# Kernel optimization log

Hardware: AMD Instinct MI355X
Metric: run time of the kernel (lower is better)

## Reference

```python
import jax, jax.numpy as jnp
import numpy as np

N = 8192
IN_F = 256
OUT_F = 128

def setup_inputs() -> dict:
    key = jax.random.key(0)
    k1, k2, k3, k4, k5 = jax.random.split(key, 5)
    adjacency_matrix = jax.random.uniform(k1, (N, N), dtype=jnp.float32)
    node_features = jax.random.normal(k2, (N, IN_F), dtype=jnp.float32)
    # nn.Linear(in_features, out_features): W is [out, in], b is [out]
    W = jax.random.normal(k3, (OUT_F, IN_F), dtype=jnp.float32) / np.sqrt(IN_F)
    b = jax.random.normal(k4, (OUT_F,), dtype=jnp.float32) * 0.01
    attn_weights = jax.random.normal(k5, (OUT_F, OUT_F), dtype=jnp.float32)
    return {"adjacency_matrix": adjacency_matrix, "node_features": node_features,
            "W": W, "b": b, "attn_weights": attn_weights}

def reference(adjacency_matrix, node_features, W, b, attn_weights):
    # h = Linear(node_features): [N, out]
    h = node_features @ W.T + b
    # bilinear scores: h @ (A @ h^T) -> [N, N]
    scores = jnp.einsum('nd,de,me->nm', h, attn_weights, h)
    attn = jax.nn.softmax(scores, axis=1)
    # weighted aggregation: [N, N] @ [N, out]
    h_agg = attn @ h
    return h_agg
```

## Files before the change

### kernel.cpp

```cpp
#include <hip/hip_runtime.h>
#include <hip/hip_bf16.h>
#include <stdint.h>


#define NN 8192
#define INF_ 256
#define D 128
#define BQ 128
#define BK 64
#define KSPLIT 8
#define KSEG (NN / KSPLIT)
#define L2E 1.44269504088896340736f

typedef __attribute__((ext_vector_type(8))) short bf16x8;
typedef __attribute__((ext_vector_type(4))) short bf16x4;
typedef __attribute__((ext_vector_type(4))) float f32x4;
typedef __attribute__((ext_vector_type(4))) unsigned int uint4v;

__global__ __launch_bounds__(256) void prep_kernel(
    const float* __restrict__ X, const float* __restrict__ W,
    const float* __restrict__ bias, const float* __restrict__ A,
    __hip_bfloat16* __restrict__ h_hi, __hip_bfloat16* __restrict__ h_lo,
    __hip_bfloat16* __restrict__ q_hi, __hip_bfloat16* __restrict__ q_lo,
    __hip_bfloat16* __restrict__ ht)
{
    __shared__ float xs[32][INF_];
    __shared__ float hs[32][D];
    const int tid  = threadIdx.x;
    const int row0 = blockIdx.x * 32;

    {
        const f32x4* Xv = (const f32x4*)(X + (size_t)row0 * INF_);
        f32x4* xsv = (f32x4*)&xs[0][0];
        #pragma unroll
        for (int i = 0; i < 8; ++i) xsv[tid + i*256] = Xv[tid + i*256];
    }
    __syncthreads();

    const int c  = tid & 127;
    const int rh = tid >> 7;

    float acc[16];
    #pragma unroll
    for (int r = 0; r < 16; ++r) acc[r] = 0.f;
    const f32x4* Wv = (const f32x4*)(W + (size_t)c * INF_);
    for (int k4 = 0; k4 < INF_/4; ++k4) {
        f32x4 w4 = Wv[k4];
        #pragma unroll
        for (int r = 0; r < 16; ++r) {
            f32x4 x4 = ((const f32x4*)&xs[rh*16 + r][0])[k4];
            acc[r] += x4[0]*w4[0] + x4[1]*w4[1] + x4[2]*w4[2] + x4[3]*w4[3];
        }
    }
    const float bc = bias[c];
    #pragma unroll
    for (int r = 0; r < 16; ++r) {
        const int row = rh*16 + r;
        const float hv = acc[r] + bc;
        hs[row][c] = hv;
        const __hip_bfloat16 hi = __float2bfloat16(hv);
        const float lo = hv - __bfloat162float(hi);
        h_hi[(size_t)(row0+row)*D + c] = hi;
        h_lo[(size_t)(row0+row)*D + c] = __float2bfloat16(lo);
        ht  [(size_t)c*NN + row0 + row] = hi;
    }
    __syncthreads();

    float acc2[16];
    #pragma unroll
    for (int r = 0; r < 16; ++r) acc2[r] = 0.f;
    for (int d4 = 0; d4 < D/4; ++d4) {
        f32x4 hv4[16];
        #pragma unroll
        for (int r = 0; r < 16; ++r) hv4[r] = ((const f32x4*)&hs[rh*16 + r][0])[d4];
        #pragma unroll
        for (int dd = 0; dd < 4; ++dd) {
            const float a = A[(size_t)(d4*4 + dd)*D + c];
            #pragma unroll
            for (int r = 0; r < 16; ++r) acc2[r] += hv4[r][dd] * a;
        }
    }
    #pragma unroll
    for (int r = 0; r < 16; ++r) {
        const int row = rh*16 + r;
        const float tv = acc2[r];
        const __hip_bfloat16 hi = __float2bfloat16(tv);
        const float lo = tv - __bfloat162float(hi);
        q_hi[(size_t)(row0+row)*D + c] = hi;
        q_lo[(size_t)(row0+row)*D + c] = __float2bfloat16(lo);
    }
}

__global__ __launch_bounds__(256, 2) void flash_kernel(
    const __hip_bfloat16* __restrict__ q_hi, const __hip_bfloat16* __restrict__ q_lo,
    const __hip_bfloat16* __restrict__ k_hi, const __hip_bfloat16* __restrict__ k_lo,
    const __hip_bfloat16* __restrict__ ht,
    float* __restrict__ opart, float* __restrict__ mpart, float* __restrict__ lpart)
{
    __shared__ __hip_bfloat16 khi[BK][136];
    __shared__ __hip_bfloat16 klo[BK][136];
    __shared__ __hip_bfloat16 vt[D][72];

    const int tid  = threadIdx.x;
    const int wave = tid >> 6;
    const int lane = tid & 63;
    const int l16  = lane & 15;
    const int quad = lane >> 4;
    const int q0    = blockIdx.x * BQ;
    const int split = blockIdx.y;
    const int jbase = split * KSEG;

    bf16x8 bqh[2][4], bql[2][4];
    #pragma unroll
    for (int it = 0; it < 2; ++it) {
        const size_t qrow = (size_t)q0 + wave*32 + it*16 + l16;
        const __hip_bfloat16* qhp = q_hi + qrow*D;
        const __hip_bfloat16* qlp = q_lo + qrow*D;
        #pragma unroll
        for (int t = 0; t < 4; ++t) {
            bqh[it][t] = *(const bf16x8*)(qhp + t*32 + quad*8);
            bql[it][t] = *(const bf16x8*)(qlp + t*32 + quad*8);
        }
    }

    f32x4 oacc[2][8];
    #pragma unroll
    for (int it = 0; it < 2; ++it)
        #pragma unroll
        for (int i = 0; i < 8; ++i) oacc[it][i] = (f32x4){0.f, 0.f, 0.f, 0.f};
    float mi[2] = {-1e30f, -1e30f}, li[2] = {0.f, 0.f};

    for (int tile = 0; tile < KSEG/BK; ++tile) {
        const int j0 = jbase + tile * BK;
        __syncthreads();
        #pragma unroll
        for (int i = 0; i < 4; ++i) {
            const int chunk = tid + i*256;
            const int r  = chunk >> 4, c8 = chunk & 15;
            *(uint4v*)(&khi[r][c8*8]) = *(const uint4v*)(k_hi + (size_t)(j0+r)*D + c8*8);
            *(uint4v*)(&klo[r][c8*8]) = *(const uint4v*)(k_lo + (size_t)(j0+r)*D + c8*8);
            const int dd = chunk >> 3, cc = chunk & 7;
            *(uint4v*)(&vt[dd][cc*8]) = *(const uint4v*)(ht + (size_t)dd*NN + j0 + cc*8);
        }
        __syncthreads();

        f32x4 st[2][4];
        #pragma unroll
        for (int jt = 0; jt < 4; ++jt) {
            #pragma unroll
            for (int t = 0; t < 4; ++t) {
                const bf16x8 ah = *(const bf16x8*)(&khi[jt*16 + l16][t*32 + quad*8]);
                const bf16x8 al = *(const bf16x8*)(&klo[jt*16 + l16][t*32 + quad*8]);
                #pragma unroll
                for (int it = 0; it < 2; ++it) {
                    f32x4 acc = (t == 0) ? (f32x4){0.f,0.f,0.f,0.f} : st[it][jt];
                    acc = __builtin_amdgcn_mfma_f32_16x16x32_bf16(ah, bql[it][t], acc, 0, 0, 0);
                    acc = __builtin_amdgcn_mfma_f32_16x16x32_bf16(al, bqh[it][t], acc, 0, 0, 0);
                    acc = __builtin_amdgcn_mfma_f32_16x16x32_bf16(ah, bqh[it][t], acc, 0, 0, 0);
                    st[it][jt] = acc;
                }
            }
        }

        bf16x8 pb[2][2];
        #pragma unroll
        for (int it = 0; it < 2; ++it) {
            float vmax = st[it][0][0];
            #pragma unroll
            for (int jt = 0; jt < 4; ++jt)
                #pragma unroll
                for (int r = 0; r < 4; ++r) vmax = fmaxf(vmax, st[it][jt][r]);
            vmax = fmaxf(vmax, __shfl_xor(vmax, 16, 64));
            vmax = fmaxf(vmax, __shfl_xor(vmax, 32, 64));
            const float mnew  = fmaxf(mi[it], vmax);
            const float alpha = exp2f((mi[it] - mnew) * L2E);
            mi[it] = mnew;
            float sum = 0.f;
            #pragma unroll
            for (int jt = 0; jt < 4; ++jt)
                #pragma unroll
                for (int r = 0; r < 4; ++r) {
                    const float pv = exp2f((st[it][jt][r] - mnew) * L2E);
                    st[it][jt][r] = pv;
                    sum += pv;
                }
            sum += __shfl_xor(sum, 16, 64);
            sum += __shfl_xor(sum, 32, 64);
            li[it] = li[it] * alpha + sum;

            #pragma unroll
            for (int r = 0; r < 4; ++r) {
                const float ar = __shfl(alpha, quad*4 + r, 64);
                #pragma unroll
                for (int dt = 0; dt < 8; ++dt) oacc[it][dt][r] *= ar;
            }
            #pragma unroll
            for (int jp = 0; jp < 2; ++jp) {
                bf16x8 f;
                #pragma unroll
                for (int r = 0; r < 4; ++r) {
                    f[r]     = __bfloat16_as_short(__float2bfloat16(st[it][2*jp  ][r]));
                    f[r + 4] = __bfloat16_as_short(__float2bfloat16(st[it][2*jp+1][r]));
                }
                pb[it][jp] = f;
            }
        }

        #pragma unroll
        for (int dt = 0; dt < 8; ++dt) {
            const __hip_bfloat16* vrow = &vt[dt*16 + l16][0];
            #pragma unroll
            for (int jp = 0; jp < 2; ++jp) {
                const bf16x4 v0 = *(const bf16x4*)(vrow + (2*jp)*16   + quad*4);
                const bf16x4 v1 = *(const bf16x4*)(vrow + (2*jp+1)*16 + quad*4);
                bf16x8 bv;
                #pragma unroll
                for (int r = 0; r < 4; ++r) { bv[r] = v0[r]; bv[r+4] = v1[r]; }
                #pragma unroll
                for (int it = 0; it < 2; ++it)
                    oacc[it][dt] = __builtin_amdgcn_mfma_f32_16x16x32_bf16(
                        pb[it][jp], bv, oacc[it][dt], 0, 0, 0);
            }
        }
    }

    float* op = opart + ((size_t)split * NN + q0 + wave*32) * D;
    #pragma unroll
    for (int it = 0; it < 2; ++it) {
        #pragma unroll
        for (int r = 0; r < 4; ++r) {
            const int m = it*16 + quad*4 + r;
            #pragma unroll
            for (int dt = 0; dt < 8; ++dt)
                op[(size_t)m*D + dt*16 + l16] = oacc[it][dt][r];
        }
        if (quad == 0) {
            mpart[(size_t)split*NN + q0 + wave*32 + it*16 + l16] = mi[it];
            lpart[(size_t)split*NN + q0 + wave*32 + it*16 + l16] = li[it];
        }
    }
}

__global__ __launch_bounds__(256) void combine_kernel(
    const float* __restrict__ opart, const float* __restrict__ mpart,
    const float* __restrict__ lpart, float* __restrict__ out)
{
    const int idx = blockIdx.x * 256 + threadIdx.x;
    const int q = idx >> 7;
    float m = -1e30f;
    #pragma unroll
    for (int s = 0; s < KSPLIT; ++s) m = fmaxf(m, mpart[(size_t)s*NN + q]);
    float z = 0.f, o = 0.f;
    #pragma unroll
    for (int s = 0; s < KSPLIT; ++s) {
        const float w = exp2f((mpart[(size_t)s*NN + q] - m) * L2E);
        z += lpart[(size_t)s*NN + q] * w;
        o += opart[(size_t)s*NN*D + idx] * w;
    }
    out[idx] = o / z;
}

extern "C" void kernel_launch(void* const* d_in, const int* in_sizes, int n_in,
                              void* d_out, int out_size, void* d_ws, size_t ws_size,
                              hipStream_t stream)
{
    const float* X = (const float*)d_in[1];
    const float* W = (const float*)d_in[2];
    const float* b = (const float*)d_in[3];
    const float* A = (const float*)d_in[4];
    float* out = (float*)d_out;

    char* ws = (char*)d_ws;
    __hip_bfloat16* h_hi = (__hip_bfloat16*)(ws);
    __hip_bfloat16* h_lo = (__hip_bfloat16*)(ws + (size_t)(2u  << 20));
    __hip_bfloat16* q_hi = (__hip_bfloat16*)(ws + (size_t)(4u  << 20));
    __hip_bfloat16* q_lo = (__hip_bfloat16*)(ws + (size_t)(6u  << 20));
    __hip_bfloat16* ht   = (__hip_bfloat16*)(ws + (size_t)(8u  << 20));
    float* opart = (float*)(ws + (size_t)(10u << 20));
    float* mpart = (float*)(ws + (size_t)(42u << 20));
    float* lpart = (float*)(ws + (size_t)(42u << 20) + (256u << 10));

    prep_kernel<<<NN/32, 256, 0, stream>>>(X, W, b, A, h_hi, h_lo, q_hi, q_lo, ht);
    flash_kernel<<<dim3(NN/BQ, KSPLIT), 256, 0, stream>>>(
        q_hi, q_lo, h_hi, h_lo, ht, opart, mpart, lpart);
    combine_kernel<<<(NN*D)/256, 256, 0, stream>>>(opart, mpart, lpart, out);
}
```

Measured before the change: 462.0 us.

## Prefetch next K/V tile into registers, permute V layout, remap block order

The flash kernel now loads the next K/V tile from global memory into registers while the current tile is being computed, hiding global load latency behind the MFMA work. The transposed V buffer is stored in a permuted column order, so each lane's PV operand becomes one contiguous 16-byte LDS read instead of two 8-byte reads plus a shuffle. The grid is flattened with split as the fastest-varying index, so neighbouring blocks share query rows, which may improve L2 locality. The cost is extra register pressure from the prefetch buffers, which could hurt occupancy at 2 blocks per CU.

```diff
diff --git a/kernel.cpp b/kernel.cpp
--- a/kernel.cpp
+++ b/kernel.cpp
@@ -10,19 +10,24 @@
 #define BK 64
 #define KSPLIT 8
 #define KSEG (NN / KSPLIT)
+#define NTILE (KSEG / BK)
 #define L2E 1.44269504088896340736f
 
 typedef __attribute__((ext_vector_type(8))) short bf16x8;
-typedef __attribute__((ext_vector_type(4))) short bf16x4;
 typedef __attribute__((ext_vector_type(4))) float f32x4;
 typedef __attribute__((ext_vector_type(4))) unsigned int uint4v;
+
+__device__ __forceinline__ int pv_perm(int g) {
+    const int jt = (g >> 4) & 3, q = (g >> 2) & 3, r = g & 3;
+    return (g & ~63) | ((jt >> 1) * 32 + q * 8 + (jt & 1) * 4 + r);
+}
 
 __global__ __launch_bounds__(256) void prep_kernel(
     const float* __restrict__ X, const float* __restrict__ W,
     const float* __restrict__ bias, const float* __restrict__ A,
     __hip_bfloat16* __restrict__ h_hi, __hip_bfloat16* __restrict__ h_lo,
     __hip_bfloat16* __restrict__ q_hi, __hip_bfloat16* __restrict__ q_lo,
-    __hip_bfloat16* __restrict__ ht)
+    __hip_bfloat16* __restrict__ htp)
 {
     __shared__ float xs[32][INF_];
     __shared__ float hs[32][D];
@@ -62,7 +67,7 @@
         const float lo = hv - __bfloat162float(hi);
         h_hi[(size_t)(row0+row)*D + c] = hi;
         h_lo[(size_t)(row0+row)*D + c] = __float2bfloat16(lo);
-        ht  [(size_t)c*NN + row0 + row] = hi;
+        htp [(size_t)c*NN + pv_perm(row0 + row)] = hi;
     }
     __syncthreads();
 
@@ -94,7 +99,7 @@
 __global__ __launch_bounds__(256, 2) void flash_kernel(
     const __hip_bfloat16* __restrict__ q_hi, const __hip_bfloat16* __restrict__ q_lo,
     const __hip_bfloat16* __restrict__ k_hi, const __hip_bfloat16* __restrict__ k_lo,
-    const __hip_bfloat16* __restrict__ ht,
+    const __hip_bfloat16* __restrict__ htp,
     float* __restrict__ opart, float* __restrict__ mpart, float* __restrict__ lpart)
 {
     __shared__ __hip_bfloat16 khi[BK][136];
@@ -106,9 +111,23 @@
     const int lane = tid & 63;
     const int l16  = lane & 15;
     const int quad = lane >> 4;
-    const int q0    = blockIdx.x * BQ;
-    const int split = blockIdx.y;
+    const int bid   = blockIdx.x;
+    const int split = bid & 7;
+    const int q0    = (bid >> 3) * BQ;
     const int jbase = split * KSEG;
+
+    int gko[4], gvo[4], lko[4], lvo[4];
+    #pragma unroll
+    for (int i = 0; i < 4; ++i) {
+        const int chunk = tid + i*256;
+        gko[i] = (chunk >> 4) * D  + (chunk & 15) * 8;
+        lko[i] = (chunk >> 4) * 136 + (chunk & 15) * 8;
+        gvo[i] = (chunk >> 3) * NN + (chunk & 7) * 8;
+        lvo[i] = (chunk >> 3) * 72 + (chunk & 7) * 8;
+    }
+    __hip_bfloat16* khi0 = &khi[0][0];
+    __hip_bfloat16* klo0 = &klo[0][0];
+    __hip_bfloat16* vt0  = &vt[0][0];
 
     bf16x8 bqh[2][4], bql[2][4];
     #pragma unroll
@@ -130,19 +149,41 @@
         for (int i = 0; i < 8; ++i) oacc[it][i] = (f32x4){0.f, 0.f, 0.f, 0.f};
     float mi[2] = {-1e30f, -1e30f}, li[2] = {0.f, 0.f};
 
-    for (int tile = 0; tile < KSEG/BK; ++tile) {
-        const int j0 = jbase + tile * BK;
+    uint4v pkh[4], pkl[4], pvv[4];
+    {
+        const __hip_bfloat16* kh = k_hi + (size_t)jbase * D;
+        const __hip_bfloat16* kl = k_lo + (size_t)jbase * D;
+        const __hip_bfloat16* vp = htp + jbase;
+        #pragma unroll
+        for (int i = 0; i < 4; ++i) {
+            pkh[i] = *(const uint4v*)(kh + gko[i]);
+            pkl[i] = *(const uint4v*)(kl + gko[i]);
+            pvv[i] = *(const uint4v*)(vp + gvo[i]);
+        }
+    }
+
+    for (int tile = 0; tile < NTILE; ++tile) {
         __syncthreads();
         #pragma unroll
         for (int i = 0; i < 4; ++i) {
-            const int chunk = tid + i*256;
-            const int r  = chunk >> 4, c8 = chunk & 15;
-            *(uint4v*)(&khi[r][c8*8]) = *(const uint4v*)(k_hi + (size_t)(j0+r)*D + c8*8);
-            *(uint4v*)(&klo[r][c8*8]) = *(const uint4v*)(k_lo + (size_t)(j0+r)*D + c8*8);
-            const int dd = chunk >> 3, cc = chunk & 7;
-            *(uint4v*)(&vt[dd][cc*8]) = *(const uint4v*)(ht + (size_t)dd*NN + j0 + cc*8);
+            *(uint4v*)(khi0 + lko[i]) = pkh[i];
+            *(uint4v*)(klo0 + lko[i]) = pkl[i];
+            *(uint4v*)(vt0  + lvo[i]) = pvv[i];
         }
         __syncthreads();
+
+        if (tile + 1 < NTILE) {
+            const size_t nb = (size_t)(jbase + (tile + 1) * BK);
+            const __hip_bfloat16* kh = k_hi + nb * D;
+            const __hip_bfloat16* kl = k_lo + nb * D;
+            const __hip_bfloat16* vp = htp + nb;
+            #pragma unroll
+            for (int i = 0; i < 4; ++i) {
+                pkh[i] = *(const uint4v*)(kh + gko[i]);
+                pkl[i] = *(const uint4v*)(kl + gko[i]);
+                pvv[i] = *(const uint4v*)(vp + gvo[i]);
+            }
+        }
 
         f32x4 st[2][4];
         #pragma unroll
@@ -211,11 +252,7 @@
             const __hip_bfloat16* vrow = &vt[dt*16 + l16][0];
             #pragma unroll
             for (int jp = 0; jp < 2; ++jp) {
-                const bf16x4 v0 = *(const bf16x4*)(vrow + (2*jp)*16   + quad*4);
-                const bf16x4 v1 = *(const bf16x4*)(vrow + (2*jp+1)*16 + quad*4);
-                bf16x8 bv;
-                #pragma unroll
-                for (int r = 0; r < 4; ++r) { bv[r] = v0[r]; bv[r+4] = v1[r]; }
+                const bf16x8 bv = *(const bf16x8*)(vrow + jp*32 + quad*8);
                 #pragma unroll
                 for (int it = 0; it < 2; ++it)
                     oacc[it][dt] = __builtin_amdgcn_mfma_f32_16x16x32_bf16(
@@ -275,13 +312,13 @@
     __hip_bfloat16* h_lo = (__hip_bfloat16*)(ws + (size_t)(2u  << 20));
     __hip_bfloat16* q_hi = (__hip_bfloat16*)(ws + (size_t)(4u  << 20));
     __hip_bfloat16* q_lo = (__hip_bfloat16*)(ws + (size_t)(6u  << 20));
-    __hip_bfloat16* ht   = (__hip_bfloat16*)(ws + (size_t)(8u  << 20));
+    __hip_bfloat16* htp  = (__hip_bfloat16*)(ws + (size_t)(8u  << 20));
     float* opart = (float*)(ws + (size_t)(10u << 20));
     float* mpart = (float*)(ws + (size_t)(42u << 20));
     float* lpart = (float*)(ws + (size_t)(42u << 20) + (256u << 10));
 
-    prep_kernel<<<NN/32, 256, 0, stream>>>(X, W, b, A, h_hi, h_lo, q_hi, q_lo, ht);
-    flash_kernel<<<dim3(NN/BQ, KSPLIT), 256, 0, stream>>>(
-        q_hi, q_lo, h_hi, h_lo, ht, opart, mpart, lpart);
+    prep_kernel<<<NN/32, 256, 0, stream>>>(X, W, b, A, h_hi, h_lo, q_hi, q_lo, htp);
+    flash_kernel<<<(NN/BQ) * KSPLIT, 256, 0, stream>>>(
+        q_hi, q_lo, h_hi, h_lo, htp, opart, mpart, lpart);
     combine_kernel<<<(NN*D)/256, 256, 0, stream>>>(opart, mpart, lpart, out);
 }
```

New measurement: 470.6 us. No clear change (+1.9%).

## Pre-swizzle K/V tiles in global memory and load via global_load_lds

Applied to the files above, without the earlier changes.

The prep kernel now writes h_hi, h_lo and the transposed h directly into per-tile, XOR-swizzled images that match the LDS layout the flash kernel reads. The flash kernel fills shared memory with direct global-to-LDS 16-byte loads, dropping the register round trip and padding, and reads V fragments as single 8-wide vectors instead of assembling them from two 4-wide loads. The grid is flattened so the eight K splits of one query block are adjacent, which may improve L2 reuse of Q. The cost is more scattered global writes in the prep kernel and reliance on the swizzle indexing being exactly right.

```diff
diff --git a/kernel.cpp b/kernel.cpp
--- a/kernel.cpp
+++ b/kernel.cpp
@@ -10,19 +10,37 @@
 #define BK 64
 #define KSPLIT 8
 #define KSEG (NN / KSPLIT)
+#define NTILE (KSEG / BK)
 #define L2E 1.44269504088896340736f
 
 typedef __attribute__((ext_vector_type(8))) short bf16x8;
-typedef __attribute__((ext_vector_type(4))) short bf16x4;
 typedef __attribute__((ext_vector_type(4))) float f32x4;
-typedef __attribute__((ext_vector_type(4))) unsigned int uint4v;
+
+__device__ __forceinline__ void gld16(const __hip_bfloat16* g, __hip_bfloat16* l) {
+    __builtin_amdgcn_global_load_lds(
+        (const __attribute__((address_space(1))) unsigned int*)(unsigned long long)(uintptr_t)g,
+        (__attribute__((address_space(3))) unsigned int*)(unsigned long long)(uintptr_t)l,
+        16, 0, 0);
+}
+
+__device__ __forceinline__ size_t k_img(int grow, int c) {
+    const int row = grow & 63;
+    return (size_t)(grow >> 6) * 8192 + row * 128 + (((c >> 3) ^ (row & 15)) * 8) + (c & 7);
+}
+
+__device__ __forceinline__ size_t v_img(int j, int c) {
+    const int jj = j & 63;
+    const int jt = (jj >> 4) & 3, q = (jj >> 2) & 3, r = jj & 3;
+    const int jp = (jt >> 1) * 32 + q * 8 + (jt & 1) * 4 + r;
+    return (size_t)(j >> 6) * 8192 + c * 64 + (((jp >> 3) ^ (c & 7)) * 8) + (jp & 7);
+}
 
 __global__ __launch_bounds__(256) void prep_kernel(
     const float* __restrict__ X, const float* __restrict__ W,
     const float* __restrict__ bias, const float* __restrict__ A,
     __hip_bfloat16* __restrict__ h_hi, __hip_bfloat16* __restrict__ h_lo,
     __hip_bfloat16* __restrict__ q_hi, __hip_bfloat16* __restrict__ q_lo,
-    __hip_bfloat16* __restrict__ ht)
+    __hip_bfloat16* __restrict__ htp)
 {
     __shared__ float xs[32][INF_];
     __shared__ float hs[32][D];
@@ -56,13 +74,14 @@
     #pragma unroll
     for (int r = 0; r < 16; ++r) {
         const int row = rh*16 + r;
+        const int grow = row0 + row;
         const float hv = acc[r] + bc;
         hs[row][c] = hv;
         const __hip_bfloat16 hi = __float2bfloat16(hv);
         const float lo = hv - __bfloat162float(hi);
-        h_hi[(size_t)(row0+row)*D + c] = hi;
-        h_lo[(size_t)(row0+row)*D + c] = __float2bfloat16(lo);
-        ht  [(size_t)c*NN + row0 + row] = hi;
+        h_hi[k_img(grow, c)] = hi;
+        h_lo[k_img(grow, c)] = __float2bfloat16(lo);
+        htp [v_img(grow, c)] = hi;
     }
     __syncthreads();
 
@@ -94,21 +113,22 @@
 __global__ __launch_bounds__(256, 2) void flash_kernel(
     const __hip_bfloat16* __restrict__ q_hi, const __hip_bfloat16* __restrict__ q_lo,
     const __hip_bfloat16* __restrict__ k_hi, const __hip_bfloat16* __restrict__ k_lo,
-    const __hip_bfloat16* __restrict__ ht,
+    const __hip_bfloat16* __restrict__ htp,
     float* __restrict__ opart, float* __restrict__ mpart, float* __restrict__ lpart)
 {
-    __shared__ __hip_bfloat16 khi[BK][136];
-    __shared__ __hip_bfloat16 klo[BK][136];
-    __shared__ __hip_bfloat16 vt[D][72];
+    __shared__ __hip_bfloat16 khi[BK*128];
+    __shared__ __hip_bfloat16 klo[BK*128];
+    __shared__ __hip_bfloat16 vt [D*64];
 
     const int tid  = threadIdx.x;
     const int wave = tid >> 6;
     const int lane = tid & 63;
     const int l16  = lane & 15;
     const int quad = lane >> 4;
-    const int q0    = blockIdx.x * BQ;
-    const int split = blockIdx.y;
-    const int jbase = split * KSEG;
+    const int bid   = blockIdx.x;
+    const int split = bid & 7;
+    const int q0    = (bid >> 3) * BQ;
+    const int tbase = split * NTILE;
 
     bf16x8 bqh[2][4], bql[2][4];
     #pragma unroll
@@ -130,17 +150,16 @@
         for (int i = 0; i < 8; ++i) oacc[it][i] = (f32x4){0.f, 0.f, 0.f, 0.f};
     float mi[2] = {-1e30f, -1e30f}, li[2] = {0.f, 0.f};
 
-    for (int tile = 0; tile < KSEG/BK; ++tile) {
-        const int j0 = jbase + tile * BK;
+    for (int tile = 0; tile < NTILE; ++tile) {
+        const size_t tb = (size_t)(tbase + tile) * 8192;
         __syncthreads();
         #pragma unroll
         for (int i = 0; i < 4; ++i) {
-            const int chunk = tid + i*256;
-            const int r  = chunk >> 4, c8 = chunk & 15;
-            *(uint4v*)(&khi[r][c8*8]) = *(const uint4v*)(k_hi + (size_t)(j0+r)*D + c8*8);
-            *(uint4v*)(&klo[r][c8*8]) = *(const uint4v*)(k_lo + (size_t)(j0+r)*D + c8*8);
-            const int dd = chunk >> 3, cc = chunk & 7;
-            *(uint4v*)(&vt[dd][cc*8]) = *(const uint4v*)(ht + (size_t)dd*NN + j0 + cc*8);
+            const int cb = (i*4 + wave) * 64;
+            const size_t ge = tb + (size_t)(cb + lane) * 8;
+            gld16(k_hi + ge, &khi[cb*8]);
+            gld16(k_lo + ge, &klo[cb*8]);
+            gld16(htp  + ge, &vt [cb*8]);
         }
         __syncthreads();
 
@@ -149,8 +168,9 @@
         for (int jt = 0; jt < 4; ++jt) {
             #pragma unroll
             for (int t = 0; t < 4; ++t) {
-                const bf16x8 ah = *(const bf16x8*)(&khi[jt*16 + l16][t*32 + quad*8]);
-                const bf16x8 al = *(const bf16x8*)(&klo[jt*16 + l16][t*32 + quad*8]);
+                const int ko = (jt*16 + l16)*128 + (((t*4 + quad) ^ l16) * 8);
+                const bf16x8 ah = *(const bf16x8*)(&khi[ko]);
+                const bf16x8 al = *(const bf16x8*)(&klo[ko]);
                 #pragma unroll
                 for (int it = 0; it < 2; ++it) {
                     f32x4 acc = (t == 0) ? (f32x4){0.f,0.f,0.f,0.f} : st[it][jt];
@@ -208,14 +228,10 @@
 
         #pragma unroll
         for (int dt = 0; dt < 8; ++dt) {
-            const __hip_bfloat16* vrow = &vt[dt*16 + l16][0];
+            const int vo = (dt*16 + l16)*64;
             #pragma unroll
             for (int jp = 0; jp < 2; ++jp) {
-                const bf16x4 v0 = *(const bf16x4*)(vrow + (2*jp)*16   + quad*4);
-                const bf16x4 v1 = *(const bf16x4*)(vrow + (2*jp+1)*16 + quad*4);
-                bf16x8 bv;
-                #pragma unroll
-                for (int r = 0; r < 4; ++r) { bv[r] = v0[r]; bv[r+4] = v1[r]; }
+                const bf16x8 bv = *(const bf16x8*)(&vt[vo + (((jp*4 + quad) ^ (l16 & 7)) * 8)]);
                 #pragma unroll
                 for (int it = 0; it < 2; ++it)
                     oacc[it][dt] = __builtin_amdgcn_mfma_f32_16x16x32_bf16(
@@ -275,13 +291,13 @@
     __hip_bfloat16* h_lo = (__hip_bfloat16*)(ws + (size_t)(2u  << 20));
     __hip_bfloat16* q_hi = (__hip_bfloat16*)(ws + (size_t)(4u  << 20));
     __hip_bfloat16* q_lo = (__hip_bfloat16*)(ws + (size_t)(6u  << 20));
-    __hip_bfloat16* ht   = (__hip_bfloat16*)(ws + (size_t)(8u  << 20));
+    __hip_bfloat16* htp  = (__hip_bfloat16*)(ws + (size_t)(8u  << 20));
     float* opart = (float*)(ws + (size_t)(10u << 20));
     float* mpart = (float*)(ws + (size_t)(42u << 20));
     float* lpart = (float*)(ws + (size_t)(42u << 20) + (256u << 10));
 
-    prep_kernel<<<NN/32, 256, 0, stream>>>(X, W, b, A, h_hi, h_lo, q_hi, q_lo, ht);
-    flash_kernel<<<dim3(NN/BQ, KSPLIT), 256, 0, stream>>>(
-        q_hi, q_lo, h_hi, h_lo, ht, opart, mpart, lpart);
+    prep_kernel<<<NN/32, 256, 0, stream>>>(X, W, b, A, h_hi, h_lo, q_hi, q_lo, htp);
+    flash_kernel<<<(NN/BQ) * KSPLIT, 256, 0, stream>>>(
+        q_hi, q_lo, h_hi, h_lo, htp, opart, mpart, lpart);
     combine_kernel<<<(NN*D)/256, 256, 0, stream>>>(opart, mpart, lpart, out);
 }
```

Measured after the change: 429.3 us. 1.08x faster.
